# Kernel optimization log

Hardware: AMD Instinct MI355X
Metric: run time of the kernel (lower is better)

## Reference

```python
import jax, jax.numpy as jnp
import numpy as np

D_MODEL = 1024
NHEAD = 16
HEAD_DIM = D_MODEL // NHEAD


def setup_inputs() -> dict:
    key = jax.random.key(0)
    ks = jax.random.split(key, 11)
    B, L, D = 4, 2048, D_MODEL
    s = 1.0 / np.sqrt(D)  # ~ torch Linear init scale
    return {
        "queries": jax.random.normal(ks[0], (B, L, D), jnp.float32),
        "keys": jax.random.normal(ks[1], (B, L, D), jnp.float32),
        "values": jax.random.normal(ks[2], (B, L, D), jnp.float32),
        "Wq": jax.random.normal(ks[3], (D, D), jnp.float32) * s,
        "bq": jnp.zeros((D,), jnp.float32),
        "Wk": jax.random.normal(ks[4], (D, D), jnp.float32) * s,
        "bk": jnp.zeros((D,), jnp.float32),
        "Wv": jax.random.normal(ks[5], (D, D), jnp.float32) * s,
        "bv": jnp.zeros((D,), jnp.float32),
        "Wo": jax.random.normal(ks[6], (D, D), jnp.float32) * s,
        "bo": jnp.zeros((D,), jnp.float32),
    }


def reference(queries, keys, values, Wq, bq, Wk, bk, Wv, bv, Wo, bo):
    B, L, D = queries.shape
    H, dh = NHEAD, HEAD_DIM
    # projections (W stored as [in, out])
    q = (queries @ Wq + bq).reshape(B, L, H, dh).transpose(0, 2, 1, 3)  # [B,H,L,dh]
    k = (keys @ Wk + bk).reshape(B, L, H, dh).transpose(0, 2, 1, 3)
    v = (values @ Wv + bv).reshape(B, L, H, dh).transpose(0, 2, 1, 3)
    scores = jnp.einsum("bhqd,bhkd->bhqk", q, k) / jnp.sqrt(jnp.float32(dh))
    attn = jax.nn.softmax(scores, axis=-1)  # dropout p=0 -> identity
    ctx = jnp.einsum("bhqk,bhkd->bhqd", attn, v)
    ctx = ctx.transpose(0, 2, 1, 3).reshape(B, L, D)
    return ctx @ Wo + bo
```

## Files before the change

### kernel.cpp

```cpp
#include <hip/hip_runtime.h>
#include <math.h>


using f32x4 = __attribute__((ext_vector_type(4))) float;
using bf16x8 = __attribute__((ext_vector_type(8))) short;

__device__ __forceinline__ unsigned short f2bf(float x) {
  union { float f; unsigned u; } v; v.f = x;
  unsigned r = v.u + 0x7fff + ((v.u >> 16) & 1);
  return (unsigned short)(r >> 16);
}

__device__ __forceinline__ void g2l16(const void* g, void* l) {
  __builtin_amdgcn_global_load_lds(
      (const __attribute__((address_space(1))) unsigned int*)g,
      (__attribute__((address_space(3))) unsigned int*)l, 16, 0, 0);
}

__global__ __launch_bounds__(256) void cvt_k(const float* __restrict__ x,
                                             short* __restrict__ y) {
  const int i4 = blockIdx.x * 256 + threadIdx.x;
  const float4 v = ((const float4*)x)[i4];
  short4 h;
  h.x = (short)f2bf(v.x);
  h.y = (short)f2bf(v.y);
  h.z = (short)f2bf(v.z);
  h.w = (short)f2bf(v.w);
  ((short4*)y)[i4] = h;
}

__global__ __launch_bounds__(256) void wt_k(const float* __restrict__ W,
                                            short* __restrict__ hiT) {
  __shared__ float t[64][65];
  const int n0 = blockIdx.x * 64, k0 = blockIdx.y * 64;
  const int tid = threadIdx.x;
  const int r = tid >> 4, c4 = (tid & 15) * 4;
#pragma unroll
  for (int i = 0; i < 4; i++) {
    const int row = r + i * 16;
    const float4 v = *(const float4*)&W[(size_t)(k0 + row) * 1024 + n0 + c4];
    t[c4 + 0][row] = v.x;
    t[c4 + 1][row] = v.y;
    t[c4 + 2][row] = v.z;
    t[c4 + 3][row] = v.w;
  }
  __syncthreads();
#pragma unroll
  for (int i = 0; i < 4; i++) {
    const int row = r + i * 16;
    short4 h;
    h.x = (short)f2bf(t[row][c4 + 0]);
    h.y = (short)f2bf(t[row][c4 + 1]);
    h.z = (short)f2bf(t[row][c4 + 2]);
    h.w = (short)f2bf(t[row][c4 + 3]);
    *(short4*)&hiT[(size_t)(n0 + row) * 1024 + k0 + c4] = h;
  }
}

template <int EPI>
__global__ __launch_bounds__(256, 2) void gemm_mfma_k(
    const short* __restrict__ A_g, const short* __restrict__ B_g,
    const float* __restrict__ bias, void* __restrict__ out0) {
  __shared__ short As[4096];
  __shared__ short Bs[4096];

  const int tid = threadIdx.x;
  const int lane = tid & 63;
  const int wave = tid >> 6;
  const int quad = lane >> 4;
  const int l16 = lane & 15;
  const int m0 = blockIdx.y * 128;
  const int n0 = blockIdx.x * 128;
  const int wm = (wave >> 1) * 64;
  const int wn = (wave & 1) * 64;

  const int srow = tid >> 2;
  const int soff = (tid & 3) * 8;

  f32x4 acc[4][4];
#pragma unroll
  for (int i = 0; i < 4; i++)
#pragma unroll
    for (int j = 0; j < 4; j++) acc[i][j] = f32x4{0.f, 0.f, 0.f, 0.f};

  for (int k0 = 0; k0 < 1024; k0 += 32) {
    __syncthreads();
#pragma unroll
    for (int i = 0; i < 2; i++) {
      const int row = srow + i * 64;
      const int lidx = row * 32 + soff;
      g2l16(&A_g[(size_t)(m0 + row) * 1024 + k0 + soff], &As[lidx]);
      g2l16(&B_g[(size_t)(n0 + row) * 1024 + k0 + soff], &Bs[lidx]);
    }
    __syncthreads();

    bf16x8 ah[4], bh[4];
#pragma unroll
    for (int t = 0; t < 4; t++) {
      ah[t] = *(const bf16x8*)&As[(wm + t * 16 + l16) * 32 + quad * 8];
      bh[t] = *(const bf16x8*)&Bs[(wn + t * 16 + l16) * 32 + quad * 8];
    }
#pragma unroll
    for (int tm = 0; tm < 4; tm++)
#pragma unroll
      for (int tn = 0; tn < 4; tn++)
        acc[tm][tn] = __builtin_amdgcn_mfma_f32_16x16x32_bf16(ah[tm], bh[tn], acc[tm][tn], 0, 0, 0);
  }

  float bz[4];
#pragma unroll
  for (int tn = 0; tn < 4; tn++) bz[tn] = bias[n0 + wn + tn * 16 + l16];

#pragma unroll
  for (int tm = 0; tm < 4; tm++) {
#pragma unroll
    for (int tn = 0; tn < 4; tn++) {
      const int n = n0 + wn + tn * 16 + l16;
#pragma unroll
      for (int r = 0; r < 4; r++) {
        const int m = m0 + wm + tm * 16 + quad * 4 + r;
        const float val = acc[tm][tn][r] + bz[tn];
        const int b = m >> 11, lrow = m & 2047;
        const int h = n >> 6, d = n & 63;
        if (EPI == 0) {
          ((short*)out0)[((size_t)(b * 16 + h) * 2048 + lrow) * 64 + d] =
              (short)f2bf(val * 0.125f);
        } else if (EPI == 1) {
          ((short*)out0)[((size_t)(b * 16 + h) * 2048 + lrow) * 64 + d] =
              (short)f2bf(val);
        } else if (EPI == 2) {
          ((short*)out0)[((size_t)(b * 16 + h) * 64 + d) * 2048 + lrow] =
              (short)f2bf(val);
        } else {
          ((float*)out0)[(size_t)m * 1024 + n] = val;
        }
      }
    }
  }
}

__global__ __launch_bounds__(256, 4) void attn3_k(const short* __restrict__ Qp,
                                                  const short* __restrict__ Kp,
                                                  const short* __restrict__ Vt,
                                                  short* __restrict__ Ctx) {
  __shared__ short Ks[64 * 72];
  __shared__ short Vs[64 * 72];
  __shared__ short Ps[128 * 72];

  const int tid = threadIdx.x;
  const int lane = tid & 63;
  const int wave = tid >> 6;
  const int quad = lane >> 4;
  const int l16 = lane & 15;
  const int bh = blockIdx.y;
  const int q0 = blockIdx.x * 128;

  const short* Kb = Kp + (size_t)bh * 2048 * 64;
  const short* Vb = Vt + (size_t)bh * 64 * 2048;

  bf16x8 qf[2][2];
#pragma unroll
  for (int s = 0; s < 2; s++) {
    const short* qp =
        Qp + ((size_t)bh * 2048 + q0 + wave * 32 + s * 16 + l16) * 64 + quad * 8;
    qf[s][0] = *(const bf16x8*)qp;
    qf[s][1] = *(const bf16x8*)(qp + 32);
  }

  bf16x8 ones;
#pragma unroll
  for (int j = 0; j < 8; j++) ones[j] = (short)0x3F80;

  f32x4 O[2][4], lacc[2];
#pragma unroll
  for (int s = 0; s < 2; s++) {
    lacc[s] = f32x4{0.f, 0.f, 0.f, 0.f};
#pragma unroll
    for (int jo = 0; jo < 4; jo++) O[s][jo] = f32x4{0.f, 0.f, 0.f, 0.f};
  }

  const int srow0 = tid >> 3, soff = (tid & 7) * 8;
  const int srow1 = (tid + 256) >> 3;

  bf16x8 kreg[2], vreg[2];
  kreg[0] = *(const bf16x8*)&Kb[(size_t)srow0 * 64 + soff];
  kreg[1] = *(const bf16x8*)&Kb[(size_t)srow1 * 64 + soff];
  vreg[0] = *(const bf16x8*)&Vb[(size_t)srow0 * 2048 + soff];
  vreg[1] = *(const bf16x8*)&Vb[(size_t)srow1 * 2048 + soff];

  for (int kt = 0; kt < 32; kt++) {
    __syncthreads();
    *(bf16x8*)&Ks[srow0 * 72 + soff] = kreg[0];
    *(bf16x8*)&Ks[srow1 * 72 + soff] = kreg[1];
    *(bf16x8*)&Vs[srow0 * 72 + soff] = vreg[0];
    *(bf16x8*)&Vs[srow1 * 72 + soff] = vreg[1];
    __syncthreads();

    if (kt < 31) {
      const int nb = (kt + 1) * 64;
      kreg[0] = *(const bf16x8*)&Kb[(size_t)(nb + srow0) * 64 + soff];
      kreg[1] = *(const bf16x8*)&Kb[(size_t)(nb + srow1) * 64 + soff];
      vreg[0] = *(const bf16x8*)&Vb[(size_t)srow0 * 2048 + nb + soff];
      vreg[1] = *(const bf16x8*)&Vb[(size_t)srow1 * 2048 + nb + soff];
    }

#pragma unroll
    for (int s = 0; s < 2; s++) {
      f32x4 sacc[4];
#pragma unroll
      for (int j = 0; j < 4; j++) sacc[j] = f32x4{0.f, 0.f, 0.f, 0.f};
#pragma unroll
      for (int c = 0; c < 2; c++)
#pragma unroll
        for (int j = 0; j < 4; j++) {
          const bf16x8 kf = *(const bf16x8*)&Ks[(j * 16 + l16) * 72 + c * 32 + quad * 8];
          sacc[j] = __builtin_amdgcn_mfma_f32_16x16x32_bf16(qf[s][c], kf, sacc[j], 0, 0, 0);
        }
#pragma unroll
      for (int j = 0; j < 4; j++)
#pragma unroll
        for (int r = 0; r < 4; r++)
          Ps[(wave * 32 + s * 16 + quad * 4 + r) * 72 + j * 16 + l16] =
              (short)f2bf(__expf(sacc[j][r]));
    }

#pragma unroll
    for (int c = 0; c < 2; c++) {
      const bf16x8 pf0 = *(const bf16x8*)&Ps[(wave * 32 + l16) * 72 + c * 32 + quad * 8];
      const bf16x8 pf1 = *(const bf16x8*)&Ps[(wave * 32 + 16 + l16) * 72 + c * 32 + quad * 8];
      lacc[0] = __builtin_amdgcn_mfma_f32_16x16x32_bf16(pf0, ones, lacc[0], 0, 0, 0);
      lacc[1] = __builtin_amdgcn_mfma_f32_16x16x32_bf16(pf1, ones, lacc[1], 0, 0, 0);
#pragma unroll
      for (int jo = 0; jo < 4; jo++) {
        const bf16x8 vf = *(const bf16x8*)&Vs[(jo * 16 + l16) * 72 + c * 32 + quad * 8];
        O[0][jo] = __builtin_amdgcn_mfma_f32_16x16x32_bf16(pf0, vf, O[0][jo], 0, 0, 0);
        O[1][jo] = __builtin_amdgcn_mfma_f32_16x16x32_bf16(pf1, vf, O[1][jo], 0, 0, 0);
      }
    }
  }

  const int b = bh >> 4, h = bh & 15;
#pragma unroll
  for (int s = 0; s < 2; s++)
#pragma unroll
    for (int r = 0; r < 4; r++) {
      const float inv_l = 1.0f / lacc[s][r];
      const size_t row = (size_t)b * 2048 + q0 + wave * 32 + s * 16 + quad * 4 + r;
#pragma unroll
      for (int jo = 0; jo < 4; jo++)
        Ctx[row * 1024 + h * 64 + jo * 16 + l16] = (short)f2bf(O[s][jo][r] * inv_l);
    }
}

extern "C" void kernel_launch(void* const* d_in, const int* in_sizes, int n_in,
                              void* d_out, int out_size, void* d_ws, size_t ws_size,
                              hipStream_t stream) {
  const float* queries = (const float*)d_in[0];
  const float* keys    = (const float*)d_in[1];
  const float* values  = (const float*)d_in[2];
  const float* Wq = (const float*)d_in[3];
  const float* bq = (const float*)d_in[4];
  const float* Wk = (const float*)d_in[5];
  const float* bk = (const float*)d_in[6];
  const float* Wv = (const float*)d_in[7];
  const float* bv = (const float*)d_in[8];
  const float* Wo = (const float*)d_in[9];
  const float* bo = (const float*)d_in[10];
  float* out = (float*)d_out;

  const size_t PLANE = (size_t)8192 * 1024 * 2;
  const size_t WPL = (size_t)1024 * 1024 * 2;

  char* p = (char*)d_ws;
  short* xbf = (short*)p;  p += PLANE;
  short* WqT = (short*)p;  p += WPL;
  short* WkT = (short*)p;  p += WPL;
  short* WvT = (short*)p;  p += WPL;
  short* WoT = (short*)p;  p += WPL;
  short* Qp  = (short*)p;  p += PLANE;
  short* Kp  = (short*)p;  p += PLANE;
  short* Vt  = (short*)p;  p += PLANE;
  short* ctx = (short*)p;  p += PLANE;

  const dim3 blk(256);
  const dim3 wgrid(16, 16);
  wt_k<<<wgrid, blk, 0, stream>>>(Wq, WqT);
  wt_k<<<wgrid, blk, 0, stream>>>(Wk, WkT);
  wt_k<<<wgrid, blk, 0, stream>>>(Wv, WvT);
  wt_k<<<wgrid, blk, 0, stream>>>(Wo, WoT);

  const dim3 ggrid(8, 64);
  const int xblocks = 8192;

  cvt_k<<<xblocks, blk, 0, stream>>>(queries, xbf);
  gemm_mfma_k<0><<<ggrid, blk, 0, stream>>>(xbf, WqT, bq, Qp);
  cvt_k<<<xblocks, blk, 0, stream>>>(keys, xbf);
  gemm_mfma_k<1><<<ggrid, blk, 0, stream>>>(xbf, WkT, bk, Kp);
  cvt_k<<<xblocks, blk, 0, stream>>>(values, xbf);
  gemm_mfma_k<2><<<ggrid, blk, 0, stream>>>(xbf, WvT, bv, Vt);

  attn3_k<<<dim3(16, 64), blk, 0, stream>>>(Qp, Kp, Vt, ctx);

  gemm_mfma_k<3><<<ggrid, blk, 0, stream>>>(ctx, WoT, bo, out);
}
```

Measured before the change: 405.5 us.

## Fuse fp32-to-bf16 input conversion into projection GEMMs and stage V transpose via LDS

```diff
diff --git a/kernel.cpp b/kernel.cpp
--- a/kernel.cpp
+++ b/kernel.cpp
@@ -15,18 +15,6 @@
   __builtin_amdgcn_global_load_lds(
       (const __attribute__((address_space(1))) unsigned int*)g,
       (__attribute__((address_space(3))) unsigned int*)l, 16, 0, 0);
-}
-
-__global__ __launch_bounds__(256) void cvt_k(const float* __restrict__ x,
-                                             short* __restrict__ y) {
-  const int i4 = blockIdx.x * 256 + threadIdx.x;
-  const float4 v = ((const float4*)x)[i4];
-  short4 h;
-  h.x = (short)f2bf(v.x);
-  h.y = (short)f2bf(v.y);
-  h.z = (short)f2bf(v.z);
-  h.w = (short)f2bf(v.w);
-  ((short4*)y)[i4] = h;
 }
 
 __global__ __launch_bounds__(256) void wt_k(const float* __restrict__ W,
@@ -57,42 +45,76 @@
   }
 }
 
-template <int EPI>
+template <int AFP32, int EPI>
 __global__ __launch_bounds__(256, 2) void gemm_mfma_k(
-    const short* __restrict__ A_g, const short* __restrict__ B_g,
+    const void* __restrict__ A_g, const short* __restrict__ B_g,
     const float* __restrict__ bias, void* __restrict__ out0) {
-  __shared__ short As[4096];
-  __shared__ short Bs[4096];
+  __shared__ short smem[64 * 144];
+  short* As = smem;
+  short* Bs = smem + 4096;
 
   const int tid = threadIdx.x;
   const int lane = tid & 63;
   const int wave = tid >> 6;
   const int quad = lane >> 4;
   const int l16 = lane & 15;
-  const int m0 = blockIdx.y * 128;
-  const int n0 = blockIdx.x * 128;
+  const int m0 = blockIdx.x * 128;
+  const int n0 = blockIdx.y * 128;
   const int wm = (wave >> 1) * 64;
   const int wn = (wave & 1) * 64;
 
   const int srow = tid >> 2;
   const int soff = (tid & 3) * 8;
+  const int arow = tid >> 1;
+  const int acol = (tid & 1) * 16;
 
   f32x4 acc[4][4];
 #pragma unroll
   for (int i = 0; i < 4; i++)
 #pragma unroll
     for (int j = 0; j < 4; j++) acc[i][j] = f32x4{0.f, 0.f, 0.f, 0.f};
+
+  float4 apre[4];
+  if (AFP32) {
+    const float* Af = (const float*)A_g;
+#pragma unroll
+    for (int j = 0; j < 4; j++)
+      apre[j] = *(const float4*)&Af[(size_t)(m0 + arow) * 1024 + acol + j * 4];
+  }
 
   for (int k0 = 0; k0 < 1024; k0 += 32) {
     __syncthreads();
+    if (AFP32) {
+      short tmp[16];
+      const float af[16] = {apre[0].x, apre[0].y, apre[0].z, apre[0].w,
+                            apre[1].x, apre[1].y, apre[1].z, apre[1].w,
+                            apre[2].x, apre[2].y, apre[2].z, apre[2].w,
+                            apre[3].x, apre[3].y, apre[3].z, apre[3].w};
+#pragma unroll
+      for (int j = 0; j < 16; j++) tmp[j] = (short)f2bf(af[j]);
+      *(bf16x8*)&As[arow * 32 + acol] = *(const bf16x8*)&tmp[0];
+      *(bf16x8*)&As[arow * 32 + acol + 8] = *(const bf16x8*)&tmp[8];
+    } else {
+#pragma unroll
+      for (int i = 0; i < 2; i++) {
+        const int row = srow + i * 64;
+        g2l16(&((const short*)A_g)[(size_t)(m0 + row) * 1024 + k0 + soff],
+              &As[row * 32 + soff]);
+      }
+    }
 #pragma unroll
     for (int i = 0; i < 2; i++) {
       const int row = srow + i * 64;
-      const int lidx = row * 32 + soff;
-      g2l16(&A_g[(size_t)(m0 + row) * 1024 + k0 + soff], &As[lidx]);
-      g2l16(&B_g[(size_t)(n0 + row) * 1024 + k0 + soff], &Bs[lidx]);
+      g2l16(&B_g[(size_t)(n0 + row) * 1024 + k0 + soff], &Bs[row * 32 + soff]);
     }
     __syncthreads();
+
+    if (AFP32 && k0 < 992) {
+      const float* Af = (const float*)A_g;
+#pragma unroll
+      for (int j = 0; j < 4; j++)
+        apre[j] = *(const float4*)&Af[(size_t)(m0 + arow) * 1024 + k0 + 32 + acol + j * 4];
+    }
 
     bf16x8 ah[4], bh[4];
 #pragma unroll
@@ -110,6 +132,38 @@
   float bz[4];
 #pragma unroll
   for (int tn = 0; tn < 4; tn++) bz[tn] = bias[n0 + wn + tn * 16 + l16];
+
+  if (EPI == 2) {
+    const int b = m0 >> 11;
+    const int lbase = m0 & 2047;
+#pragma unroll
+    for (int half = 0; half < 2; half++) {
+      __syncthreads();
+      if ((wave & 1) == half) {
+#pragma unroll
+        for (int tm = 0; tm < 4; tm++)
+#pragma unroll
+          for (int tn = 0; tn < 4; tn++)
+#pragma unroll
+            for (int r = 0; r < 4; r++) {
+              const int nl = tn * 16 + l16;
+              const int ml = wm + tm * 16 + quad * 4 + r;
+              smem[nl * 144 + ml] = (short)f2bf(acc[tm][tn][r] + bz[tn]);
+            }
+      }
+      __syncthreads();
+      const int h = (n0 >> 6) + half;
+#pragma unroll
+      for (int j = 0; j < 4; j++) {
+        const int c = tid + j * 256;
+        const int d = c >> 4;
+        const int mo = (c & 15) * 8;
+        *(bf16x8*)&((short*)out0)[((size_t)((b * 16 + h) * 64 + d)) * 2048 + lbase + mo] =
+            *(const bf16x8*)&smem[d * 144 + mo];
+      }
+    }
+    return;
+  }
 
 #pragma unroll
   for (int tm = 0; tm < 4; tm++) {
@@ -128,9 +182,6 @@
         } else if (EPI == 1) {
           ((short*)out0)[((size_t)(b * 16 + h) * 2048 + lrow) * 64 + d] =
               (short)f2bf(val);
-        } else if (EPI == 2) {
-          ((short*)out0)[((size_t)(b * 16 + h) * 64 + d) * 2048 + lrow] =
-              (short)f2bf(val);
         } else {
           ((float*)out0)[(size_t)m * 1024 + n] = val;
         }
@@ -219,9 +270,11 @@
 #pragma unroll
       for (int j = 0; j < 4; j++)
 #pragma unroll
-        for (int r = 0; r < 4; r++)
+        for (int r = 0; r < 4; r++) {
+          const float e = __expf(sacc[j][r]);
           Ps[(wave * 32 + s * 16 + quad * 4 + r) * 72 + j * 16 + l16] =
-              (short)f2bf(__expf(sacc[j][r]));
+              (short)(__float_as_uint(e) >> 16);
+        }
     }
 
 #pragma unroll
@@ -272,7 +325,6 @@
   const size_t WPL = (size_t)1024 * 1024 * 2;
 
   char* p = (char*)d_ws;
-  short* xbf = (short*)p;  p += PLANE;
   short* WqT = (short*)p;  p += WPL;
   short* WkT = (short*)p;  p += WPL;
   short* WvT = (short*)p;  p += WPL;
@@ -289,17 +341,13 @@
   wt_k<<<wgrid, blk, 0, stream>>>(Wv, WvT);
   wt_k<<<wgrid, blk, 0, stream>>>(Wo, WoT);
 
-  const dim3 ggrid(8, 64);
-  const int xblocks = 8192;
-
-  cvt_k<<<xblocks, blk, 0, stream>>>(queries, xbf);
-  gemm_mfma_k<0><<<ggrid, blk, 0, stream>>>(xbf, WqT, bq, Qp);
-  cvt_k<<<xblocks, blk, 0, stream>>>(keys, xbf);
-  gemm_mfma_k<1><<<ggrid, blk, 0, stream>>>(xbf, WkT, bk, Kp);
-  cvt_k<<<xblocks, blk, 0, stream>>>(values, xbf);
-  gemm_mfma_k<2><<<ggrid, blk, 0, stream>>>(xbf, WvT, bv, Vt);
+  const dim3 ggrid(64, 8);
+
+  gemm_mfma_k<1, 0><<<ggrid, blk, 0, stream>>>(queries, WqT, bq, Qp);
+  gemm_mfma_k<1, 1><<<ggrid, blk, 0, stream>>>(keys,    WkT, bk, Kp);
+  gemm_mfma_k<1, 2><<<ggrid, blk, 0, stream>>>(values,  WvT, bv, Vt);
 
   attn3_k<<<dim3(16, 64), blk, 0, stream>>>(Qp, Kp, Vt, ctx);
 
-  gemm_mfma_k<3><<<ggrid, blk, 0, stream>>>(ctx, WoT, bo, out);
-}
+  gemm_mfma_k<0, 3><<<ggrid, blk, 0, stream>>>(ctx, WoT, bo, out);
+}
```

After: 407.8 us. About the same (+0.6%).
